# Optimization experiments

Hardware: AMD Instinct MI355X
Metric: run time of the kernel (lower is better)

The kernel has to match this reference:

```python
import jax, jax.numpy as jnp
import numpy as np
from functools import partial

B, S = 4, 4096
IN_FEATURES = 4096   # == padded_in (power of 2, no padding path)
OUT_FEATURES = 4096  # == padded_out
NUM_FACTORS = 12     # ceil(log2(4096))


def setup_inputs() -> dict:
    key = jax.random.key(0)
    k_x, k_f = jax.random.split(key)
    x = jax.random.normal(k_x, (B, S, IN_FEATURES), dtype=jnp.float32)
    # matches torch.randn(num_blocks, 2, 2) * 0.01 init, stacked over factors
    factors = jax.random.normal(
        k_f, (NUM_FACTORS, IN_FEATURES // 2, 2, 2), dtype=jnp.float32) * 0.01
    alpha = jnp.ones((1,), dtype=jnp.float32)
    return {"x": x, "factors": factors, "alpha": alpha}


def _butterfly(x_flat, factors, alpha):
    # x_flat: [M, N]; factors: [F, N//2, 2, 2]
    M, N = x_flat.shape

    def step(r, f):
        rb = r.reshape(M, N // 2, 2)
        rb = jnp.einsum('mnb,nbc->mnc', rb, f)
        return rb.reshape(M, N), None

    out, _ = jax.lax.scan(step, x_flat, factors)
    return out[:, :OUT_FEATURES] * alpha  # alpha broadcasts; bias is None


def reference(x, factors, alpha):
    batch_dims = x.shape[:-1]
    x_flat = x.reshape(-1, IN_FEATURES)  # in_features == padded_in -> no pad
    out = _butterfly(x_flat, factors, alpha)
    return out.reshape(*batch_dims, OUT_FEATURES)
```

## Files before the change

### kernel.cpp

```cpp
#include <hip/hip_runtime.h>

#define ROWS        16384
#define N           4096
#define COLS4       1024
#define NFACT       12
#define NPAIRS      2048
#define ROWS_PER_BLOCK 64

__global__ __launch_bounds__(256) void butterfly_fused_kernel(
    const float4* __restrict__ x,
    const float4* __restrict__ factors,
    const float*  __restrict__ alpha,
    float4* __restrict__ out)
{
    const int c  = blockIdx.x * blockDim.x + threadIdx.x;
    const int r0 = blockIdx.y * ROWS_PER_BLOCK;
    const int p0 = 2 * c;
    const int p1 = 2 * c + 1;

    float a00 = 1.f, a01 = 0.f, a10 = 0.f, a11 = 1.f;
    float b00 = 1.f, b01 = 0.f, b10 = 0.f, b11 = 1.f;

#pragma unroll
    for (int f = 0; f < NFACT; ++f) {
        float4 F0 = factors[f * NPAIRS + p0];
        float4 F1 = factors[f * NPAIRS + p1];

        float n00 = a00 * F0.x + a01 * F0.z;
        float n01 = a00 * F0.y + a01 * F0.w;
        float n10 = a10 * F0.x + a11 * F0.z;
        float n11 = a10 * F0.y + a11 * F0.w;
        a00 = n00; a01 = n01; a10 = n10; a11 = n11;

        float m00 = b00 * F1.x + b01 * F1.z;
        float m01 = b00 * F1.y + b01 * F1.w;
        float m10 = b10 * F1.x + b11 * F1.z;
        float m11 = b10 * F1.y + b11 * F1.w;
        b00 = m00; b01 = m01; b10 = m10; b11 = m11;
    }

    const float al = alpha[0];
    a00 *= al; a01 *= al; a10 *= al; a11 *= al;
    b00 *= al; b01 *= al; b10 *= al; b11 *= al;

#pragma unroll 8
    for (int i = 0; i < ROWS_PER_BLOCK; ++i) {
        const size_t idx = (size_t)(r0 + i) * COLS4 + c;
        float4 v = x[idx];
        float4 o;
        o.x = v.x * a00 + v.y * a10;
        o.y = v.x * a01 + v.y * a11;
        o.z = v.z * b00 + v.w * b10;
        o.w = v.z * b01 + v.w * b11;
        out[idx] = o;
    }
}

extern "C" void kernel_launch(void* const* d_in, const int* in_sizes, int n_in,
                              void* d_out, int out_size, void* d_ws, size_t ws_size,
                              hipStream_t stream) {
    const float4* x       = (const float4*)d_in[0];
    const float4* factors = (const float4*)d_in[1];
    const float*  alpha   = (const float*)d_in[2];
    float4* out           = (float4*)d_out;

    dim3 grid(COLS4 / 256, ROWS / ROWS_PER_BLOCK);
    dim3 block(256);
    butterfly_fused_kernel<<<grid, block, 0, stream>>>(x, factors, alpha, out);
}
```

Before: 452.5 us.

## Precompute combined butterfly factors in separate kernel and stream with nontemporal access

Moves the per-column product of the 12 factor matrices into a small pre-kernel that writes the combined 2x2 blocks to the workspace. The streaming kernel then reads only those blocks, uses fewer rows per block (more blocks), fully unrolls the row loop, and uses nontemporal loads and stores. The aim is to stop every block from recomputing the factor chain and to raise memory-level parallelism on a bandwidth-bound pass. It adds a second launch and a dependency on the workspace buffer.

```diff
diff --git a/kernel.cpp b/kernel.cpp
--- a/kernel.cpp
+++ b/kernel.cpp
@@ -5,66 +5,67 @@
 #define COLS4       1024
 #define NFACT       12
 #define NPAIRS      2048
-#define ROWS_PER_BLOCK 64
+#define RPB         16
 
-__global__ __launch_bounds__(256) void butterfly_fused_kernel(
-    const float4* __restrict__ x,
-    const float4* __restrict__ factors,
-    const float*  __restrict__ alpha,
-    float4* __restrict__ out)
+typedef float f32x4 __attribute__((ext_vector_type(4)));
+
+__global__ __launch_bounds__(256) void combine_factors_kernel(
+    const f32x4* __restrict__ factors,
+    const float* __restrict__ alpha,
+    f32x4* __restrict__ C)
+{
+    const int p = blockIdx.x * blockDim.x + threadIdx.x;
+    float a00 = 1.f, a01 = 0.f, a10 = 0.f, a11 = 1.f;
+#pragma unroll
+    for (int f = 0; f < NFACT; ++f) {
+        f32x4 F = factors[f * NPAIRS + p];
+        float n00 = a00 * F.x + a01 * F.z;
+        float n01 = a00 * F.y + a01 * F.w;
+        float n10 = a10 * F.x + a11 * F.z;
+        float n11 = a10 * F.y + a11 * F.w;
+        a00 = n00; a01 = n01; a10 = n10; a11 = n11;
+    }
+    const float al = alpha[0];
+    f32x4 r;
+    r.x = a00 * al; r.y = a01 * al; r.z = a10 * al; r.w = a11 * al;
+    C[p] = r;
+}
+
+__global__ __launch_bounds__(256) void butterfly_stream_kernel(
+    const f32x4* __restrict__ x,
+    const f32x4* __restrict__ C,
+    f32x4* __restrict__ out)
 {
     const int c  = blockIdx.x * blockDim.x + threadIdx.x;
-    const int r0 = blockIdx.y * ROWS_PER_BLOCK;
-    const int p0 = 2 * c;
-    const int p1 = 2 * c + 1;
+    const int r0 = blockIdx.y * RPB;
 
-    float a00 = 1.f, a01 = 0.f, a10 = 0.f, a11 = 1.f;
-    float b00 = 1.f, b01 = 0.f, b10 = 0.f, b11 = 1.f;
+    const f32x4 A  = C[2 * c];
+    const f32x4 Bm = C[2 * c + 1];
 
 #pragma unroll
-    for (int f = 0; f < NFACT; ++f) {
-        float4 F0 = factors[f * NPAIRS + p0];
-        float4 F1 = factors[f * NPAIRS + p1];
-
-        float n00 = a00 * F0.x + a01 * F0.z;
-        float n01 = a00 * F0.y + a01 * F0.w;
-        float n10 = a10 * F0.x + a11 * F0.z;
-        float n11 = a10 * F0.y + a11 * F0.w;
-        a00 = n00; a01 = n01; a10 = n10; a11 = n11;
-
-        float m00 = b00 * F1.x + b01 * F1.z;
-        float m01 = b00 * F1.y + b01 * F1.w;
-        float m10 = b10 * F1.x + b11 * F1.z;
-        float m11 = b10 * F1.y + b11 * F1.w;
-        b00 = m00; b01 = m01; b10 = m10; b11 = m11;
-    }
-
-    const float al = alpha[0];
-    a00 *= al; a01 *= al; a10 *= al; a11 *= al;
-    b00 *= al; b01 *= al; b10 *= al; b11 *= al;
-
-#pragma unroll 8
-    for (int i = 0; i < ROWS_PER_BLOCK; ++i) {
+    for (int i = 0; i < RPB; ++i) {
         const size_t idx = (size_t)(r0 + i) * COLS4 + c;
-        float4 v = x[idx];
-        float4 o;
-        o.x = v.x * a00 + v.y * a10;
-        o.y = v.x * a01 + v.y * a11;
-        o.z = v.z * b00 + v.w * b10;
-        o.w = v.z * b01 + v.w * b11;
-        out[idx] = o;
+        f32x4 v = __builtin_nontemporal_load(&x[idx]);
+        f32x4 o;
+        o.x = v.x * A.x  + v.y * A.z;
+        o.y = v.x * A.y  + v.y * A.w;
+        o.z = v.z * Bm.x + v.w * Bm.z;
+        o.w = v.z * Bm.y + v.w * Bm.w;
+        __builtin_nontemporal_store(o, &out[idx]);
     }
 }
 
 extern "C" void kernel_launch(void* const* d_in, const int* in_sizes, int n_in,
                               void* d_out, int out_size, void* d_ws, size_t ws_size,
                               hipStream_t stream) {
-    const float4* x       = (const float4*)d_in[0];
-    const float4* factors = (const float4*)d_in[1];
-    const float*  alpha   = (const float*)d_in[2];
-    float4* out           = (float4*)d_out;
+    const f32x4* x       = (const f32x4*)d_in[0];
+    const f32x4* factors = (const f32x4*)d_in[1];
+    const float* alpha   = (const float*)d_in[2];
+    f32x4* out           = (f32x4*)d_out;
+    f32x4* C             = (f32x4*)d_ws;
 
-    dim3 grid(COLS4 / 256, ROWS / ROWS_PER_BLOCK);
-    dim3 block(256);
-    butterfly_fused_kernel<<<grid, block, 0, stream>>>(x, factors, alpha, out);
+    combine_factors_kernel<<<NPAIRS / 256, 256, 0, stream>>>(factors, alpha, C);
+
+    dim3 grid(COLS4 / 256, ROWS / RPB);
+    butterfly_stream_kernel<<<grid, 256, 0, stream>>>(x, C, out);
 }
```

After: 435.9 us. 3.7% less time.
